# Kernel optimization log

Hardware: AMD Instinct MI355X
Metric: run time of the kernel (lower is better)

## Reference

```python
import math
import jax, jax.numpy as jnp
import numpy as np

SEQ, BATCH, D_MODEL, HEADS = 2048, 2, 1024, 16
D_K = D_MODEL // HEADS


def setup_inputs() -> dict:
    key = jax.random.key(0)
    ks = jax.random.split(key, 11)
    s = 1.0 / math.sqrt(D_MODEL)
    inp = {
        "q": jax.random.normal(ks[0], (SEQ, BATCH, D_MODEL), jnp.float32),
        "k": jax.random.normal(ks[1], (SEQ, BATCH, D_MODEL), jnp.float32),
        "v": jax.random.normal(ks[2], (SEQ, BATCH, D_MODEL), jnp.float32),
        "Wq": jax.random.normal(ks[3], (D_MODEL, D_MODEL), jnp.float32) * s,
        "bq": jnp.zeros((D_MODEL,), jnp.float32),
        "Wk": jax.random.normal(ks[4], (D_MODEL, D_MODEL), jnp.float32) * s,
        "bk": jnp.zeros((D_MODEL,), jnp.float32),
        "Wv": jax.random.normal(ks[5], (D_MODEL, D_MODEL), jnp.float32) * s,
        "bv": jnp.zeros((D_MODEL,), jnp.float32),
        "Wo": jax.random.normal(ks[6], (D_MODEL, D_MODEL), jnp.float32) * s,
        "bo": jnp.zeros((D_MODEL,), jnp.float32),
    }
    return inp


def _proj(x, W, b):
    # [S,B,D] @ [D, H*Dk] -> [S,B,H,Dk]
    y = jnp.einsum('sbd,de->sbe', x, W) + b
    return y.reshape(x.shape[0], x.shape[1], HEADS, D_K)


def reference(q, k, v, Wq, bq, Wk, bk, Wv, bv, Wo, bo):
    scale = 1.0 / math.sqrt(D_K)
    query = _proj(q, Wq, bq)            # [i,b,h,d]
    key_ = _proj(k, Wk, bk)             # [j,b,h,d]
    value = _proj(v, Wv, bv)            # [j,b,h,d]
    scores = jnp.einsum('ibhd,jbhd->ijbh', query, key_) * scale
    attn = jax.nn.softmax(scores, axis=1)  # softmax over key axis j (dim=1)
    x = jnp.einsum('ijbh,jbhd->ibhd', attn, value)
    x = x.reshape(SEQ, BATCH, D_MODEL)
    return jnp.einsum('sbd,de->sbe', x, Wo) + bo
```

## Files before the change

### kernel.cpp

```cpp
#include <hip/hip_runtime.h>
#include <hip/hip_bf16.h>


typedef __attribute__((ext_vector_type(8))) short bf16x8;
typedef __attribute__((ext_vector_type(4))) float f32x4;

constexpr int SEQ   = 2048;
constexpr int BATCH = 2;
constexpr int DM    = 1024;
constexpr int DK    = 64;
constexpr int MR    = SEQ * BATCH;
constexpr int SST   = BATCH * DM;
constexpr int HD    = SEQ * DK;

#define CE_SCALE 0.18033688011112042592f

__device__ __forceinline__ unsigned pkbf(float a, float b) {
    __hip_bfloat162 h = __float22bfloat162_rn(float2{a, b});
    union { __hip_bfloat162 h2; unsigned u; } cv;
    cv.h2 = h;
    return cv.u;
}

__device__ __forceinline__ f32x4 mfma16(bf16x8 a, bf16x8 b, f32x4 c) {
    return __builtin_amdgcn_mfma_f32_16x16x32_bf16(a, b, c, 0, 0, 0);
}

__device__ __forceinline__ void gl16(const unsigned short* g, unsigned short* l) {
    __builtin_amdgcn_global_load_lds(
        (const __attribute__((address_space(1))) void*)g,
        (__attribute__((address_space(3))) void*)l, 16, 0, 0);
}

__global__ __launch_bounds__(256)
void wt_prep_all(const float* __restrict__ w0, const float* __restrict__ w1,
                 const float* __restrict__ w2, const float* __restrict__ w3,
                 unsigned short* __restrict__ o0, unsigned short* __restrict__ o1,
                 unsigned short* __restrict__ o2, unsigned short* __restrict__ o3)
{
    const int z = blockIdx.z;
    const float* W = (z == 0) ? w0 : (z == 1) ? w1 : (z == 2) ? w2 : w3;
    unsigned short* Wt = (z == 0) ? o0 : (z == 1) ? o1 : (z == 2) ? o2 : o3;
    const float sc = (z == 0) ? CE_SCALE : 1.0f;

    const int t = threadIdx.x;
    const int e = blockIdx.x * 64 + (t & 63);
    const int dq = blockIdx.y * 256 + (t >> 6) * 64;
    unsigned short* orow = Wt + (size_t)e * DM + dq;
#pragma unroll
    for (int c = 0; c < 8; ++c) {
        float f[8];
#pragma unroll
        for (int j = 0; j < 8; ++j)
            f[j] = W[(size_t)(dq + c * 8 + j) * DM + e] * sc;
        uint4 u = { pkbf(f[0], f[1]), pkbf(f[2], f[3]),
                    pkbf(f[4], f[5]), pkbf(f[6], f[7]) };
        *(uint4*)(orow + c * 8) = u;
    }
}

__global__ __launch_bounds__(256)
void qkv_cast(const float* __restrict__ qa, const float* __restrict__ ka,
              const float* __restrict__ va,
              unsigned short* __restrict__ Qb, unsigned short* __restrict__ Kb,
              unsigned short* __restrict__ Vb)
{
    const int z = blockIdx.y;
    const float* src = (z == 0) ? qa : (z == 1) ? ka : va;
    unsigned short* dst = (z == 0) ? Qb : (z == 1) ? Kb : Vb;
    const size_t i = ((size_t)blockIdx.x * 256 + threadIdx.x) * 8;
    float4 f0 = *(const float4*)(src + i);
    float4 f1 = *(const float4*)(src + i + 4);
    uint4 u = { pkbf(f0.x, f0.y), pkbf(f0.z, f0.w),
                pkbf(f1.x, f1.y), pkbf(f1.z, f1.w) };
    *(uint4*)(dst + i) = u;
}

__global__ __launch_bounds__(256)
void gemm_qkv_b(const unsigned short* __restrict__ Qb,
                const unsigned short* __restrict__ Kb,
                const unsigned short* __restrict__ Vb,
                const unsigned short* __restrict__ wq,
                const unsigned short* __restrict__ wk,
                const unsigned short* __restrict__ wv,
                const float* __restrict__ bq, const float* __restrict__ bk,
                const float* __restrict__ bv,
                unsigned short* __restrict__ Qh, unsigned short* __restrict__ Kh,
                unsigned short* __restrict__ Vtp)
{
    constexpr int K = 1024;
    __shared__ unsigned short smem[16384];
    unsigned short* As0 = smem;
    unsigned short* As1 = smem + 4096;
    unsigned short* Bs0 = smem + 8192;
    unsigned short* Bs1 = smem + 12288;

    const int z = blockIdx.z;
    const unsigned short* Ab = (z == 0) ? Qb : (z == 1) ? Kb : Vb;
    const unsigned short* Bt = (z == 0) ? wq : (z == 1) ? wk : wv;
    const float* bias = (z == 0) ? bq : (z == 1) ? bk : bv;
    const float bscale = (z == 0) ? CE_SCALE : 1.0f;

    const int l = blockIdx.x + 8 * blockIdx.y;
    const int xcd = l & 7, jj0 = l >> 3;
    const int bm = xcd * 4 + (jj0 >> 3);
    const int bn = jj0 & 7;

    const int tid = threadIdx.x;
    const int wave = tid >> 6, lane = tid & 63;
    const int wr = wave >> 1, wc = wave & 1;
    const int lrow = lane & 15, g = lane >> 4;
    const int gr = lane & 15, gc = (lane >> 4) * 8;

    const unsigned short* aRow0 = Ab + (size_t)(bm * 128 + wave * 32 + gr) * K + gc;
    const unsigned short* aRow1 = aRow0 + (size_t)16 * K;
    const unsigned short* bRow0 = Bt + (size_t)(bn * 128 + wave * 32 + gr) * K + gc;
    const unsigned short* bRow1 = bRow0 + (size_t)16 * K;

    f32x4 acc[4][4] = {};

    auto stage0 = [&](int k0) {
        gl16(aRow0 + k0, As0 + (2 * wave) * 512);
        gl16(aRow1 + k0, As0 + (2 * wave + 1) * 512);
        gl16(bRow0 + k0, Bs0 + (2 * wave) * 512);
        gl16(bRow1 + k0, Bs0 + (2 * wave + 1) * 512);
    };
    auto stage1 = [&](int k0) {
        gl16(aRow0 + k0, As1 + (2 * wave) * 512);
        gl16(aRow1 + k0, As1 + (2 * wave + 1) * 512);
        gl16(bRow0 + k0, Bs1 + (2 * wave) * 512);
        gl16(bRow1 + k0, Bs1 + (2 * wave + 1) * 512);
    };
    auto loadFrag = [&](bf16x8 (&af)[4], bf16x8 (&bfr)[4],
                        const unsigned short* as, const unsigned short* bs) {
#pragma unroll
        for (int i = 0; i < 4; ++i)
            af[i] = *(const bf16x8*)&as[(wr * 4 + i) * 512 + lane * 8];
#pragma unroll
        for (int j = 0; j < 4; ++j)
            bfr[j] = *(const bf16x8*)&bs[(wc * 4 + j) * 512 + lane * 8];
    };
    auto domfma = [&](bf16x8 (&af)[4], bf16x8 (&bfr)[4]) {
        __builtin_amdgcn_s_setprio(1);
#pragma unroll
        for (int i = 0; i < 4; ++i)
#pragma unroll
            for (int j = 0; j < 4; ++j)
                acc[i][j] = mfma16(af[i], bfr[j], acc[i][j]);
        __builtin_amdgcn_s_setprio(0);
    };

    stage0(0);
    stage1(32);

#pragma unroll 1
    for (int k0 = 0; k0 < 960; k0 += 64) {
        asm volatile("s_waitcnt vmcnt(4)" ::: "memory");
        __builtin_amdgcn_s_barrier();
        {
            bf16x8 af[4], bfr[4];
            loadFrag(af, bfr, As0, Bs0);
            asm volatile("s_waitcnt lgkmcnt(0)" ::: "memory");
            __builtin_amdgcn_sched_barrier(0);
            __builtin_amdgcn_s_barrier();
            stage0(k0 + 64);
            domfma(af, bfr);
        }
        asm volatile("s_waitcnt vmcnt(4)" ::: "memory");
        __builtin_amdgcn_s_barrier();
        {
            bf16x8 af[4], bfr[4];
            loadFrag(af, bfr, As1, Bs1);
            asm volatile("s_waitcnt lgkmcnt(0)" ::: "memory");
            __builtin_amdgcn_sched_barrier(0);
            __builtin_amdgcn_s_barrier();
            stage1(k0 + 96);
            domfma(af, bfr);
        }
    }
    {
        asm volatile("s_waitcnt vmcnt(4)" ::: "memory");
        __builtin_amdgcn_s_barrier();
        bf16x8 af[4], bfr[4];
        loadFrag(af, bfr, As0, Bs0);
        domfma(af, bfr);
    }
    {
        asm volatile("s_waitcnt vmcnt(0)" ::: "memory");
        __builtin_amdgcn_s_barrier();
        bf16x8 af[4], bfr[4];
        loadFrag(af, bfr, As1, Bs1);
        domfma(af, bfr);
    }

    __syncthreads();
#pragma unroll 1
    for (int p = 0; p < 2; ++p) {
        if (wc == p) {
#pragma unroll
            for (int j = 0; j < 4; ++j) {
                const int col = bn * 128 + p * 64 + j * 16 + lrow;
                const float bb = bias[col] * bscale;
#pragma unroll
                for (int i = 0; i < 4; ++i)
#pragma unroll
                    for (int r = 0; r < 4; ++r) {
                        const int lr = wr * 64 + i * 16 + 4 * g + r;
                        smem[lr * 72 + j * 16 + lrow] =
                            (unsigned short)(pkbf(acc[i][j][r] + bb, 0.f) & 0xffffu);
                    }
            }
        }
        __syncthreads();
        if (z != 2) {
            unsigned short* C = (z == 0) ? Qh : Kh;
            const int lr = tid >> 1, half = tid & 1;
            const int s = bm * 64 + (lr >> 1), b = lr & 1, h = bn * 2 + p;
            const unsigned short* src = &smem[lr * 72 + half * 32];
            unsigned short* dst = C + (size_t)(b * 16 + h) * HD + (size_t)s * 64 + half * 32;
#pragma unroll
            for (int w2 = 0; w2 < 4; ++w2)
                *(uint4*)(dst + w2 * 8) = *(const uint4*)(src + w2 * 8);
        } else {
            const int d = tid >> 2, b = (tid >> 1) & 1, sh = tid & 1;
            const int h = bn * 2 + p;
            unsigned tmp[16];
#pragma unroll
            for (int t2 = 0; t2 < 16; ++t2) {
                const int p0 = 2 * t2, p1 = p0 + 1;
                const int r5a = ((p0 >> 2) & 1) * 16 + (p0 >> 3) * 4 + (p0 & 3);
                const int r5b = ((p1 >> 2) & 1) * 16 + (p1 >> 3) * 4 + (p1 & 3);
                const unsigned va = smem[(64 * sh + 2 * r5a + b) * 72 + d];
                const unsigned vb2 = smem[(64 * sh + 2 * r5b + b) * 72 + d];
                tmp[t2] = va | (vb2 << 16);
            }
            unsigned short* dst = Vtp + (size_t)(b * 16 + h) * HD + (size_t)d * SEQ
                                      + bm * 64 + sh * 32;
#pragma unroll
            for (int w2 = 0; w2 < 4; ++w2) {
                uint4 u = { tmp[4 * w2], tmp[4 * w2 + 1], tmp[4 * w2 + 2], tmp[4 * w2 + 3] };
                *(uint4*)(dst + w2 * 8) = u;
            }
        }
        __syncthreads();
    }
}

__global__ __launch_bounds__(256)
void attn_mfma(const unsigned short* __restrict__ Qh,
               const unsigned short* __restrict__ Kh,
               const unsigned short* __restrict__ Vtp,
               unsigned short* __restrict__ Xp)
{
    __shared__ unsigned short lds[24576];

    const int tid = threadIdx.x;
    const int fid = blockIdx.x;
    const int xcd = fid & 7, idx = fid >> 3;
    const int bh = xcd * 4 + (idx >> 4);
    const int qt = idx & 15;

    const int wave = tid >> 6, lane = tid & 63;
    const int lrow = lane & 15, g = lane >> 4;
    const int s7 = lrow & 7;
    const int q0w = qt * 128 + wave * 32;

    const unsigned short* qb = Qh + (size_t)bh * HD;
    const unsigned short* kb = Kh + (size_t)bh * HD;
    const unsigned short* vb = Vtp + (size_t)bh * HD;

    const int r8 = lane >> 3, c8 = lane & 7;
    const unsigned short* ksrcA = kb + (size_t)(wave * 16 + r8) * 64 + (c8 ^ r8) * 8;
    const unsigned short* ksrcB = ksrcA + 8 * 64;
    const unsigned short* vsrcA = vb + (size_t)(wave * 16 + r8) * SEQ + (c8 ^ r8) * 8;
    const unsigned short* vsrcB = vsrcA + 8 * SEQ;

    auto stage = [&](int t, unsigned short* base) {
        const size_t ko = (size_t)t * 4096;
        const size_t vo = (size_t)t * 64;
        gl16(ksrcA + ko, base + wave * 1024);
        gl16(ksrcB + ko, base + wave * 1024 + 512);
        gl16(vsrcA + vo, base + 4096 + wave * 1024);
        gl16(vsrcB + vo, base + 4096 + wave * 1024 + 512);
    };

    bf16x8 bq[2][2];
#pragma unroll
    for (int qi = 0; qi < 2; ++qi)
#pragma unroll
        for (int dc = 0; dc < 2; ++dc)
            bq[qi][dc] = *(const bf16x8*)(qb + (size_t)(q0w + qi * 16 + lrow) * 64
                                             + dc * 32 + g * 8);

    bf16x8 aones;
    {
        union { uint4 u; bf16x8 v; } cv;
        const unsigned o2 = (lrow == 0) ? 0x3F803F80u : 0u;
        cv.u = make_uint4(o2, o2, o2, o2);
        aones = cv.v;
    }

    f32x4 oacc[4][2] = {};
    f32x4 lacc[2] = {};

    const int off0 = lrow * 64 + ((g ^ s7) * 8);
    const int off1 = lrow * 64 + (((4 + g) ^ s7) * 8);

    stage(0, lds);
    stage(1, lds + 8192);

    int bcur = 0;
#pragma unroll 1
    for (int t = 0; t < 32; ++t) {
        unsigned short* kbuf = lds + bcur * 8192;
        unsigned short* vbuf = kbuf + 4096;

        if (t < 31) { asm volatile("s_waitcnt vmcnt(4)" ::: "memory"); }
        else        { asm volatile("s_waitcnt vmcnt(0)" ::: "memory"); }
        __builtin_amdgcn_s_barrier();

        bf16x8 ak[4][2], av[4][2];
#pragma unroll
        for (int kt = 0; kt < 4; ++kt) {
            ak[kt][0] = *(const bf16x8*)(kbuf + kt * 1024 + off0);
            ak[kt][1] = *(const bf16x8*)(kbuf + kt * 1024 + off1);
        }
#pragma unroll
        for (int dt = 0; dt < 4; ++dt) {
            av[dt][0] = *(const bf16x8*)(vbuf + dt * 1024 + off0);
            av[dt][1] = *(const bf16x8*)(vbuf + dt * 1024 + off1);
        }
        asm volatile("s_waitcnt lgkmcnt(0)" ::: "memory");
        __builtin_amdgcn_sched_barrier(0);
        __builtin_amdgcn_s_barrier();

        if (t + 2 < 32) {
            int bn3 = bcur + 2; if (bn3 >= 3) bn3 -= 3;
            stage(t + 2, lds + bn3 * 8192);
        }

        uint4 pbu[2][2];
        __builtin_amdgcn_s_setprio(1);
#pragma unroll
        for (int qi = 0; qi < 2; ++qi) {
#pragma unroll
            for (int kt = 0; kt < 4; ++kt) {
                f32x4 s = { 0.f, 0.f, 0.f, 0.f };
                s = mfma16(ak[kt][0], bq[qi][0], s);
                s = mfma16(ak[kt][1], bq[qi][1], s);
                const float p0 = __builtin_amdgcn_exp2f(s[0]);
                const float p1 = __builtin_amdgcn_exp2f(s[1]);
                const float p2 = __builtin_amdgcn_exp2f(s[2]);
                const float p3 = __builtin_amdgcn_exp2f(s[3]);
                const unsigned lo = pkbf(p0, p1);
                const unsigned hi = pkbf(p2, p3);
                if (kt & 1) { pbu[kt >> 1][qi].z = lo; pbu[kt >> 1][qi].w = hi; }
                else        { pbu[kt >> 1][qi].x = lo; pbu[kt >> 1][qi].y = hi; }
            }
        }

#pragma unroll
        for (int kc = 0; kc < 2; ++kc) {
#pragma unroll
            for (int dt = 0; dt < 4; ++dt)
#pragma unroll
                for (int qi = 0; qi < 2; ++qi) {
                    union { uint4 u; bf16x8 v; } cv;
                    cv.u = pbu[kc][qi];
                    oacc[dt][qi] = mfma16(av[dt][kc], cv.v, oacc[dt][qi]);
                }
#pragma unroll
            for (int qi = 0; qi < 2; ++qi) {
                union { uint4 u; bf16x8 v; } cv;
                cv.u = pbu[kc][qi];
                lacc[qi] = mfma16(aones, cv.v, lacc[qi]);
            }
        }
        __builtin_amdgcn_s_setprio(0);

        bcur = (bcur + 1 == 3) ? 0 : bcur + 1;
    }

    const float ls0 = __shfl(lacc[0][0], lrow);
    const float ls1 = __shfl(lacc[1][0], lrow);
    const float inv0 = 1.0f / ls0, inv1 = 1.0f / ls1;

    __builtin_amdgcn_s_barrier();

    unsigned short (*osh)[72] = (unsigned short (*)[72])(lds + wave * 32 * 72);
#pragma unroll
    for (int qi = 0; qi < 2; ++qi) {
        const float inv = qi ? inv1 : inv0;
#pragma unroll
        for (int dt = 0; dt < 4; ++dt) {
            const int d0 = dt * 16 + 4 * g;
            const unsigned u0 = pkbf(oacc[dt][qi][0] * inv, oacc[dt][qi][1] * inv);
            const unsigned u1 = pkbf(oacc[dt][qi][2] * inv, oacc[dt][qi][3] * inv);
            *(unsigned*)&osh[qi * 16 + lrow][d0] = u0;
            *(unsigned*)&osh[qi * 16 + lrow][d0 + 2] = u1;
        }
    }
    const int ql = lane >> 1;
    const int dh = (lane & 1) * 32;
    unsigned short* xrow = Xp + (size_t)(q0w + ql) * SST + bh * 64 + dh;
#pragma unroll
    for (int c = 0; c < 4; ++c) {
        uint4 vv = *(const uint4*)&osh[ql][dh + c * 8];
        *(uint4*)(xrow + c * 8) = vv;
    }
}

__global__ __launch_bounds__(256)
void gemm_out(const unsigned short* __restrict__ Xp,
              const unsigned short* __restrict__ WtO,
              const float* __restrict__ bias, float* __restrict__ out)
{
    constexpr int K = 1024, N = 1024;
    __shared__ unsigned short smem[12288];
    unsigned short* As0 = smem;
    unsigned short* As1 = smem + 4096;
    unsigned short* Bs0 = smem + 8192;
    unsigned short* Bs1 = smem + 10240;

    const int l = blockIdx.x + 16 * blockIdx.y;
    const int xcd = l & 7, jj0 = l >> 3;
    const int bm = xcd * 4 + (jj0 >> 4);
    const int bn = jj0 & 15;

    const int tid = threadIdx.x;
    const int wave = tid >> 6, lane = tid & 63;
    const int wr = wave >> 1, wc = wave & 1;
    const int lrow = lane & 15, g = lane >> 4;
    const int gr = lane & 15, gc = (lane >> 4) * 8;

    const unsigned short* aRow0 = Xp + (size_t)(bm * 128 + wave * 32 + gr) * K + gc;
    const unsigned short* aRow1 = aRow0 + (size_t)16 * K;
    const unsigned short* bRow0 = WtO + (size_t)(bn * 64 + wave * 16 + gr) * K + gc;

    f32x4 acc[4][2] = {};

    auto stage0 = [&](int k0) {
        gl16(aRow0 + k0, As0 + (2 * wave) * 512);
        gl16(aRow1 + k0, As0 + (2 * wave + 1) * 512);
        gl16(bRow0 + k0, Bs0 + wave * 512);
    };
    auto stage1 = [&](int k0) {
        gl16(aRow0 + k0, As1 + (2 * wave) * 512);
        gl16(aRow1 + k0, As1 + (2 * wave + 1) * 512);
        gl16(bRow0 + k0, Bs1 + wave * 512);
    };
    auto loadFrag = [&](bf16x8 (&af)[4], bf16x8 (&bfr)[2],
                        const unsigned short* as, const unsigned short* bs) {
#pragma unroll
        for (int i = 0; i < 4; ++i)
            af[i] = *(const bf16x8*)&as[(wr * 4 + i) * 512 + lane * 8];
#pragma unroll
        for (int j = 0; j < 2; ++j)
            bfr[j] = *(const bf16x8*)&bs[(wc * 2 + j) * 512 + lane * 8];
    };
    auto domfma = [&](bf16x8 (&af)[4], bf16x8 (&bfr)[2]) {
        __builtin_amdgcn_s_setprio(1);
#pragma unroll
        for (int i = 0; i < 4; ++i)
#pragma unroll
            for (int j = 0; j < 2; ++j)
                acc[i][j] = mfma16(af[i], bfr[j], acc[i][j]);
        __builtin_amdgcn_s_setprio(0);
    };

    stage0(0);
    stage1(32);

#pragma unroll 1
    for (int k0 = 0; k0 < 960; k0 += 64) {
        asm volatile("s_waitcnt vmcnt(3)" ::: "memory");
        __builtin_amdgcn_s_barrier();
        {
            bf16x8 af[4], bfr[2];
            loadFrag(af, bfr, As0, Bs0);
            asm volatile("s_waitcnt lgkmcnt(0)" ::: "memory");
            __builtin_amdgcn_sched_barrier(0);
            __builtin_amdgcn_s_barrier();
            stage0(k0 + 64);
            domfma(af, bfr);
        }
        asm volatile("s_waitcnt vmcnt(3)" ::: "memory");
        __builtin_amdgcn_s_barrier();
        {
            bf16x8 af[4], bfr[2];
            loadFrag(af, bfr, As1, Bs1);
            asm volatile("s_waitcnt lgkmcnt(0)" ::: "memory");
            __builtin_amdgcn_sched_barrier(0);
            __builtin_amdgcn_s_barrier();
            stage1(k0 + 96);
            domfma(af, bfr);
        }
    }
    {
        asm volatile("s_waitcnt vmcnt(3)" ::: "memory");
        __builtin_amdgcn_s_barrier();
        bf16x8 af[4], bfr[2];
        loadFrag(af, bfr, As0, Bs0);
        domfma(af, bfr);
    }
    {
        asm volatile("s_waitcnt vmcnt(0)" ::: "memory");
        __builtin_amdgcn_s_barrier();
        bf16x8 af[4], bfr[2];
        loadFrag(af, bfr, As1, Bs1);
        domfma(af, bfr);
    }

    __syncthreads();
    float* LF = (float*)smem;
#pragma unroll 1
    for (int q2 = 0; q2 < 2; ++q2) {
        if (wr == q2) {
#pragma unroll
            for (int j = 0; j < 2; ++j) {
                const int c = wc * 32 + j * 16 + lrow;
                const float bb = bias[bn * 64 + c];
#pragma unroll
                for (int i = 0; i < 4; ++i)
#pragma unroll
                    for (int r = 0; r < 4; ++r)
                        LF[(i * 16 + 4 * g + r) * 68 + c] = acc[i][j][r] + bb;
            }
        }
        __syncthreads();
        {
            const int lr = tid >> 2, c0 = (tid & 3) * 16;
            const float* srcp = &LF[lr * 68 + c0];
            float* dst = out + (size_t)(bm * 128 + q2 * 64 + lr) * N + bn * 64 + c0;
#pragma unroll
            for (int w2 = 0; w2 < 4; ++w2)
                *(float4*)(dst + w2 * 4) = *(const float4*)(srcp + w2 * 4);
        }
        __syncthreads();
    }
}

extern "C" void kernel_launch(void* const* d_in, const int* in_sizes, int n_in,
                              void* d_out, int out_size, void* d_ws, size_t ws_size,
                              hipStream_t stream) {
    (void)in_sizes; (void)n_in; (void)out_size; (void)ws_size;

    const float* q  = (const float*)d_in[0];
    const float* k  = (const float*)d_in[1];
    const float* v  = (const float*)d_in[2];
    const float* Wq = (const float*)d_in[3];
    const float* bq = (const float*)d_in[4];
    const float* Wk = (const float*)d_in[5];
    const float* bk = (const float*)d_in[6];
    const float* Wv = (const float*)d_in[7];
    const float* bv = (const float*)d_in[8];
    const float* Wo = (const float*)d_in[9];
    const float* bo = (const float*)d_in[10];
    float* out = (float*)d_out;

    unsigned short* ws = (unsigned short*)d_ws;
    const size_t WSZ = (size_t)DM * DM;
    const size_t MSZ = (size_t)MR * DM;
    unsigned short* WtQ = ws;
    unsigned short* WtK = ws + WSZ;
    unsigned short* WtV = ws + 2 * WSZ;
    unsigned short* WtO = ws + 3 * WSZ;
    unsigned short* Qb  = ws + 4 * WSZ;
    unsigned short* Kb  = Qb + MSZ;
    unsigned short* Vb  = Kb + MSZ;
    unsigned short* Qh  = Vb + MSZ;
    unsigned short* Kh  = Qh + MSZ;
    unsigned short* Vtp = Kh + MSZ;
    unsigned short* Xp  = Vtp + MSZ;

    const dim3 blk(256);

    wt_prep_all<<<dim3(16, 4, 4), blk, 0, stream>>>(Wq, Wk, Wv, Wo, WtQ, WtK, WtV, WtO);

    qkv_cast<<<dim3(2048, 3), blk, 0, stream>>>(q, k, v, Qb, Kb, Vb);

    gemm_qkv_b<<<dim3(8, 32, 3), blk, 0, stream>>>(Qb, Kb, Vb, WtQ, WtK, WtV,
                                                   bq, bk, bv, Qh, Kh, Vtp);

    attn_mfma<<<dim3(512), blk, 0, stream>>>(Qh, Kh, Vtp, Xp);

    gemm_out<<<dim3(16, 32), blk, 0, stream>>>(Xp, WtO, bo, out);
}
```

Measured before the change: 146.1 us.

## Enlarge QKV projection GEMM tiles to 256x256 with 512 threads and triple-buffered LDS

The QKV projection GEMM moves from 128x128 tiles with 4 waves to 256x256 tiles with 8 waves, each wave computing a 128x64 sub-tile. The LDS prefetch goes from a double buffer to a three-slot ring with a prefetch distance of two stages. The epilogue is reworked to write four 64-row chunks per block into the Q/K head layout and the transposed V layout. The aim is higher arithmetic intensity per byte loaded and fewer global reloads. The cost is only 192 blocks, which underfills the 256 CUs, plus more registers and 96KB of LDS per block.

```diff
diff --git a/kernel.cpp b/kernel.cpp
--- a/kernel.cpp
+++ b/kernel.cpp
@@ -76,166 +76,144 @@
     *(uint4*)(dst + i) = u;
 }
 
-__global__ __launch_bounds__(256)
-void gemm_qkv_b(const unsigned short* __restrict__ Qb,
-                const unsigned short* __restrict__ Kb,
-                const unsigned short* __restrict__ Vb,
-                const unsigned short* __restrict__ wq,
-                const unsigned short* __restrict__ wk,
-                const unsigned short* __restrict__ wv,
-                const float* __restrict__ bq, const float* __restrict__ bk,
-                const float* __restrict__ bv,
-                unsigned short* __restrict__ Qh, unsigned short* __restrict__ Kh,
-                unsigned short* __restrict__ Vtp)
+__global__ __launch_bounds__(512)
+void qkv256(const unsigned short* __restrict__ Qb,
+            const unsigned short* __restrict__ Kb,
+            const unsigned short* __restrict__ Vb,
+            const unsigned short* __restrict__ wq,
+            const unsigned short* __restrict__ wk,
+            const unsigned short* __restrict__ wv,
+            const float* __restrict__ bq, const float* __restrict__ bk,
+            const float* __restrict__ bv,
+            unsigned short* __restrict__ Qh, unsigned short* __restrict__ Kh,
+            unsigned short* __restrict__ Vtp)
 {
     constexpr int K = 1024;
-    __shared__ unsigned short smem[16384];
-    unsigned short* As0 = smem;
-    unsigned short* As1 = smem + 4096;
-    unsigned short* Bs0 = smem + 8192;
-    unsigned short* Bs1 = smem + 12288;
-
-    const int z = blockIdx.z;
+    constexpr int SLOT = 16384;
+    __shared__ unsigned short smem[49152];
+
+    const int z = blockIdx.y;
     const unsigned short* Ab = (z == 0) ? Qb : (z == 1) ? Kb : Vb;
     const unsigned short* Bt = (z == 0) ? wq : (z == 1) ? wk : wv;
     const float* bias = (z == 0) ? bq : (z == 1) ? bk : bv;
     const float bscale = (z == 0) ? CE_SCALE : 1.0f;
 
-    const int l = blockIdx.x + 8 * blockIdx.y;
-    const int xcd = l & 7, jj0 = l >> 3;
-    const int bm = xcd * 4 + (jj0 >> 3);
-    const int bn = jj0 & 7;
+    const int bx = blockIdx.x;
+    const int xcd = bx & 7, j64 = bx >> 3;
+    const int bm = xcd * 2 + (j64 >> 2);
+    const int bn = j64 & 3;
 
     const int tid = threadIdx.x;
     const int wave = tid >> 6, lane = tid & 63;
-    const int wr = wave >> 1, wc = wave & 1;
+    const int wr = wave >> 2, wcn = wave & 3;
     const int lrow = lane & 15, g = lane >> 4;
     const int gr = lane & 15, gc = (lane >> 4) * 8;
 
-    const unsigned short* aRow0 = Ab + (size_t)(bm * 128 + wave * 32 + gr) * K + gc;
-    const unsigned short* aRow1 = aRow0 + (size_t)16 * K;
-    const unsigned short* bRow0 = Bt + (size_t)(bn * 128 + wave * 32 + gr) * K + gc;
-    const unsigned short* bRow1 = bRow0 + (size_t)16 * K;
-
-    f32x4 acc[4][4] = {};
-
-    auto stage0 = [&](int k0) {
-        gl16(aRow0 + k0, As0 + (2 * wave) * 512);
-        gl16(aRow1 + k0, As0 + (2 * wave + 1) * 512);
-        gl16(bRow0 + k0, Bs0 + (2 * wave) * 512);
-        gl16(bRow1 + k0, Bs0 + (2 * wave + 1) * 512);
+    const unsigned short* aU0 = Ab + (size_t)(bm * 256 + wave * 32 + gr) * K + gc;
+    const unsigned short* aU1 = aU0 + (size_t)16 * K;
+    const unsigned short* bU0 = Bt + (size_t)(bn * 256 + wave * 32 + gr) * K + gc;
+    const unsigned short* bU1 = bU0 + (size_t)16 * K;
+
+    f32x4 acc[8][4] = {};
+
+    auto stage = [&](int t, int slot) {
+        unsigned short* As = smem + slot * SLOT;
+        unsigned short* Bs = As + 8192;
+        const int k0 = t * 32;
+        gl16(aU0 + k0, As + (2 * wave) * 512);
+        gl16(aU1 + k0, As + (2 * wave + 1) * 512);
+        gl16(bU0 + k0, Bs + (2 * wave) * 512);
+        gl16(bU1 + k0, Bs + (2 * wave + 1) * 512);
     };
-    auto stage1 = [&](int k0) {
-        gl16(aRow0 + k0, As1 + (2 * wave) * 512);
-        gl16(aRow1 + k0, As1 + (2 * wave + 1) * 512);
-        gl16(bRow0 + k0, Bs1 + (2 * wave) * 512);
-        gl16(bRow1 + k0, Bs1 + (2 * wave + 1) * 512);
-    };
-    auto loadFrag = [&](bf16x8 (&af)[4], bf16x8 (&bfr)[4],
-                        const unsigned short* as, const unsigned short* bs) {
-#pragma unroll
-        for (int i = 0; i < 4; ++i)
-            af[i] = *(const bf16x8*)&as[(wr * 4 + i) * 512 + lane * 8];
+
+    stage(0, 0);
+    stage(1, 1);
+
+    int bcur = 0;
+#pragma unroll 1
+    for (int t = 0; t < 32; ++t) {
+        const unsigned short* As = smem + bcur * SLOT;
+        const unsigned short* Bs = As + 8192;
+
+        if (t < 31) { asm volatile("s_waitcnt vmcnt(4)" ::: "memory"); }
+        else        { asm volatile("s_waitcnt vmcnt(0)" ::: "memory"); }
+        __builtin_amdgcn_s_barrier();
+
+        bf16x8 af[8], bfr[4];
+#pragma unroll
+        for (int i = 0; i < 8; ++i)
+            af[i] = *(const bf16x8*)&As[(wr * 8 + i) * 512 + lane * 8];
 #pragma unroll
         for (int j = 0; j < 4; ++j)
-            bfr[j] = *(const bf16x8*)&bs[(wc * 4 + j) * 512 + lane * 8];
-    };
-    auto domfma = [&](bf16x8 (&af)[4], bf16x8 (&bfr)[4]) {
+            bfr[j] = *(const bf16x8*)&Bs[(wcn * 4 + j) * 512 + lane * 8];
+        asm volatile("s_waitcnt lgkmcnt(0)" ::: "memory");
+        __builtin_amdgcn_sched_barrier(0);
+        __builtin_amdgcn_s_barrier();
+
+        if (t + 2 < 32) {
+            int ns = bcur + 2; if (ns >= 3) ns -= 3;
+            stage(t + 2, ns);
+        }
+
         __builtin_amdgcn_s_setprio(1);
 #pragma unroll
-        for (int i = 0; i < 4; ++i)
+        for (int i = 0; i < 8; ++i)
 #pragma unroll
             for (int j = 0; j < 4; ++j)
                 acc[i][j] = mfma16(af[i], bfr[j], acc[i][j]);
         __builtin_amdgcn_s_setprio(0);
-    };
-
-    stage0(0);
-    stage1(32);
-
-#pragma unroll 1
-    for (int k0 = 0; k0 < 960; k0 += 64) {
-        asm volatile("s_waitcnt vmcnt(4)" ::: "memory");
-        __builtin_amdgcn_s_barrier();
-        {
-            bf16x8 af[4], bfr[4];
-            loadFrag(af, bfr, As0, Bs0);
-            asm volatile("s_waitcnt lgkmcnt(0)" ::: "memory");
-            __builtin_amdgcn_sched_barrier(0);
-            __builtin_amdgcn_s_barrier();
-            stage0(k0 + 64);
-            domfma(af, bfr);
-        }
-        asm volatile("s_waitcnt vmcnt(4)" ::: "memory");
-        __builtin_amdgcn_s_barrier();
-        {
-            bf16x8 af[4], bfr[4];
-            loadFrag(af, bfr, As1, Bs1);
-            asm volatile("s_waitcnt lgkmcnt(0)" ::: "memory");
-            __builtin_amdgcn_sched_barrier(0);
-            __builtin_amdgcn_s_barrier();
-            stage1(k0 + 96);
-            domfma(af, bfr);
-        }
-    }
-    {
-        asm volatile("s_waitcnt vmcnt(4)" ::: "memory");
-        __builtin_amdgcn_s_barrier();
-        bf16x8 af[4], bfr[4];
-        loadFrag(af, bfr, As0, Bs0);
-        domfma(af, bfr);
-    }
-    {
-        asm volatile("s_waitcnt vmcnt(0)" ::: "memory");
-        __builtin_amdgcn_s_barrier();
-        bf16x8 af[4], bfr[4];
-        loadFrag(af, bfr, As1, Bs1);
-        domfma(af, bfr);
-    }
-
+
+        bcur = (bcur + 1 == 3) ? 0 : bcur + 1;
+    }
+
+    constexpr int LBS = 258;
     __syncthreads();
 #pragma unroll 1
-    for (int p = 0; p < 2; ++p) {
-        if (wc == p) {
+    for (int rq = 0; rq < 4; ++rq) {
+        if (wr == (rq >> 1)) {
+            const int i0 = (rq & 1) * 4;
 #pragma unroll
             for (int j = 0; j < 4; ++j) {
-                const int col = bn * 128 + p * 64 + j * 16 + lrow;
-                const float bb = bias[col] * bscale;
-#pragma unroll
-                for (int i = 0; i < 4; ++i)
+                const int c = wcn * 64 + j * 16 + lrow;
+                const float bb = bias[bn * 256 + c] * bscale;
+#pragma unroll
+                for (int i2 = 0; i2 < 4; ++i2)
 #pragma unroll
                     for (int r = 0; r < 4; ++r) {
-                        const int lr = wr * 64 + i * 16 + 4 * g + r;
-                        smem[lr * 72 + j * 16 + lrow] =
-                            (unsigned short)(pkbf(acc[i][j][r] + bb, 0.f) & 0xffffu);
+                        const int lr = i2 * 16 + 4 * g + r;
+                        smem[lr * LBS + c] =
+                            (unsigned short)(pkbf(acc[i0 + i2][j][r] + bb, 0.f) & 0xffffu);
                     }
             }
         }
         __syncthreads();
         if (z != 2) {
             unsigned short* C = (z == 0) ? Qh : Kh;
-            const int lr = tid >> 1, half = tid & 1;
-            const int s = bm * 64 + (lr >> 1), b = lr & 1, h = bn * 2 + p;
-            const unsigned short* src = &smem[lr * 72 + half * 32];
-            unsigned short* dst = C + (size_t)(b * 16 + h) * HD + (size_t)s * 64 + half * 32;
+            const int lr = tid >> 3, ch = (tid >> 1) & 3, hf = tid & 1;
+            const int grow = bm * 256 + rq * 64 + lr;
+            const int s = grow >> 1, b = grow & 1, h = bn * 4 + ch;
+            const unsigned short* src = &smem[lr * LBS + ch * 64 + hf * 32];
+            unsigned short* dst = C + (size_t)(b * 16 + h) * HD + (size_t)s * 64 + hf * 32;
 #pragma unroll
             for (int w2 = 0; w2 < 4; ++w2)
                 *(uint4*)(dst + w2 * 8) = *(const uint4*)(src + w2 * 8);
         } else {
-            const int d = tid >> 2, b = (tid >> 1) & 1, sh = tid & 1;
-            const int h = bn * 2 + p;
+            const int ch = tid >> 7, d = (tid >> 1) & 63, b = tid & 1;
+            const int h = bn * 4 + ch;
             unsigned tmp[16];
 #pragma unroll
-            for (int t2 = 0; t2 < 16; ++t2) {
-                const int p0 = 2 * t2, p1 = p0 + 1;
+            for (int m = 0; m < 16; ++m) {
+                const int p0 = 2 * m, p1 = p0 + 1;
                 const int r5a = ((p0 >> 2) & 1) * 16 + (p0 >> 3) * 4 + (p0 & 3);
                 const int r5b = ((p1 >> 2) & 1) * 16 + (p1 >> 3) * 4 + (p1 & 3);
-                const unsigned va = smem[(64 * sh + 2 * r5a + b) * 72 + d];
-                const unsigned vb2 = smem[(64 * sh + 2 * r5b + b) * 72 + d];
-                tmp[t2] = va | (vb2 << 16);
+                const unsigned va  = smem[(2 * r5a + b) * LBS + ch * 64 + d];
+                const unsigned vb2 = smem[(2 * r5b + b) * LBS + ch * 64 + d];
+                tmp[m] = va | (vb2 << 16);
             }
+            const int sbase = bm * 128 + rq * 32;
+            const int st = sbase >> 6, kc = (sbase >> 5) & 1;
             unsigned short* dst = Vtp + (size_t)(b * 16 + h) * HD + (size_t)d * SEQ
-                                      + bm * 64 + sh * 32;
+                                      + st * 64 + kc * 32;
 #pragma unroll
             for (int w2 = 0; w2 < 4; ++w2) {
                 uint4 u = { tmp[4 * w2], tmp[4 * w2 + 1], tmp[4 * w2 + 2], tmp[4 * w2 + 3] };
@@ -573,16 +551,15 @@
     unsigned short* Vtp = Kh + MSZ;
     unsigned short* Xp  = Vtp + MSZ;
 
-    const dim3 blk(256);
-
-    wt_prep_all<<<dim3(16, 4, 4), blk, 0, stream>>>(Wq, Wk, Wv, Wo, WtQ, WtK, WtV, WtO);
-
-    qkv_cast<<<dim3(2048, 3), blk, 0, stream>>>(q, k, v, Qb, Kb, Vb);
-
-    gemm_qkv_b<<<dim3(8, 32, 3), blk, 0, stream>>>(Qb, Kb, Vb, WtQ, WtK, WtV,
-                                                   bq, bk, bv, Qh, Kh, Vtp);
-
-    attn_mfma<<<dim3(512), blk, 0, stream>>>(Qh, Kh, Vtp, Xp);
-
-    gemm_out<<<dim3(16, 32), blk, 0, stream>>>(Xp, WtO, bo, out);
-}
+    wt_prep_all<<<dim3(16, 4, 4), dim3(256), 0, stream>>>(Wq, Wk, Wv, Wo,
+                                                          WtQ, WtK, WtV, WtO);
+
+    qkv_cast<<<dim3(2048, 3), dim3(256), 0, stream>>>(q, k, v, Qb, Kb, Vb);
+
+    qkv256<<<dim3(64, 3), dim3(512), 0, stream>>>(Qb, Kb, Vb, WtQ, WtK, WtV,
+                                                  bq, bk, bv, Qh, Kh, Vtp);
+
+    attn_mfma<<<dim3(512), dim3(256), 0, stream>>>(Qh, Kh, Vtp, Xp);
+
+    gemm_out<<<dim3(16, 32), dim3(256), 0, stream>>>(Xp, WtO, bo, out);
+}
```

Result: slower. 156.0 us (+6.7%).
